# Kernel optimization log

Measured on AMD Instinct MI355X. Metric: run time of the kernel, lower is better.

Reference implementation:

```python
import jax, jax.numpy as jnp
import numpy as np

N, E, G = 50000, 800000, 64
DIN, H, DOUT = 128, 64, 1
T = 3  # AttentiveFP message-passing timesteps
NEG_SLOPE = 0.2


def setup_inputs() -> dict:
    key = jax.random.key(0)
    ks = jax.random.split(key, 16)
    s = 0.05
    return {
        "x": jax.random.normal(ks[0], (N, DIN), jnp.float32),
        "edge_index": jax.random.randint(ks[1], (2, E), 0, N),
        "batch": jnp.sort(jax.random.randint(ks[2], (N,), 0, G)),
        "W_in": jax.random.normal(ks[3], (DIN, H), jnp.float32) * s,
        "b_in": jnp.zeros((H,), jnp.float32),
        "a_att": jax.random.normal(ks[4], (2 * H,), jnp.float32) * s,
        "Wi": jax.random.normal(ks[5], (H, 3 * H), jnp.float32) * s,
        "Wh": jax.random.normal(ks[6], (H, 3 * H), jnp.float32) * s,
        "bi": jnp.zeros((3 * H,), jnp.float32),
        "bh": jnp.zeros((3 * H,), jnp.float32),
        "W1": jax.random.normal(ks[7], (2 * H, H), jnp.float32) * s,
        "b1": jnp.zeros((H,), jnp.float32),
        "W2": jax.random.normal(ks[8], (H, DOUT), jnp.float32) * s,
        "b2": jnp.zeros((DOUT,), jnp.float32),
    }


def _segment_softmax(scores, seg, n):
    m = jax.ops.segment_max(scores, seg, num_segments=n)
    e = jnp.exp(scores - m[seg])
    z = jax.ops.segment_sum(e, seg, num_segments=n)
    return e / (z[seg] + 1e-16)


def reference(x, edge_index, batch, W_in, b_in, a_att, Wi, Wh, bi, bh, W1, b1, W2, b2):
    src, dst = edge_index[0], edge_index[1]
    # input projection
    h = jax.nn.relu(x @ W_in + b_in)  # [N, H]
    for _ in range(T):
        # attention-weighted message passing (AttentiveFP style)
        h_src, h_dst = h[src], h[dst]                      # [E, H] gathers
        score = jax.nn.leaky_relu(
            h_src @ a_att[:H] + h_dst @ a_att[H:], NEG_SLOPE)  # [E]
        alpha = _segment_softmax(score, dst, N)            # softmax over incoming edges
        m = jax.ops.segment_sum(alpha[:, None] * h_src, dst, num_segments=N)  # [N, H]
        # GRU cell update: h = GRU(m, h)
        gi = m @ Wi + bi
        gh = h @ Wh + bh
        r = jax.nn.sigmoid(gi[:, :H] + gh[:, :H])
        z = jax.nn.sigmoid(gi[:, H:2 * H] + gh[:, H:2 * H])
        n = jnp.tanh(gi[:, 2 * H:] + r * gh[:, 2 * H:])
        h = (1.0 - z) * n + z * h
    # graph readout: mean || max pooling -> [G, 2H]
    cnt = jax.ops.segment_sum(jnp.ones((N,), h.dtype), batch, num_segments=G)
    meanp = jax.ops.segment_sum(h, batch, num_segments=G) / jnp.maximum(cnt, 1.0)[:, None]
    maxp = jax.ops.segment_max(h, batch, num_segments=G)
    maxp = jnp.where(jnp.isfinite(maxp), maxp, 0.0)
    g = jnp.concatenate([meanp, maxp], axis=-1)  # [G, 2H]
    # dropout is identity in eval mode; MLP head
    g = jax.nn.relu(g @ W1 + b1)
    return g @ W2 + b2  # [G, DOUT]
```

## Files before the change

kernel.cpp:

```cpp
#include <hip/hip_runtime.h>
#include <math.h>

#define DIN 128
#define HD 64
#define NEG 0.2f

typedef short s16x8 __attribute__((ext_vector_type(8)));
typedef float f32x4 __attribute__((ext_vector_type(4)));

__device__ __forceinline__ float sigmoidf_(float x) { return 1.f / (1.f + __expf(-x)); }
__device__ __forceinline__ float tanhf_(float x)    { return 2.f / (1.f + __expf(-2.f*x)) - 1.f; }

__device__ __forceinline__ void split2(float a, float b, unsigned& dh, unsigned& dl) {
  unsigned ha = __float_as_uint(a) & 0xffff0000u;
  unsigned hb = __float_as_uint(b) & 0xffff0000u;
  float ra = a - __uint_as_float(ha);
  float rb = b - __uint_as_float(hb);
  unsigned la = __float_as_uint(ra) & 0xffff0000u;
  unsigned lb = __float_as_uint(rb) & 0xffff0000u;
  dh = (ha >> 16) | hb;
  dl = (la >> 16) | lb;
}

__device__ __forceinline__ unsigned pack2rne(float a, float b) {
  unsigned ua = __float_as_uint(a); ua += 0x7fffu + ((ua >> 16) & 1u);
  unsigned ub = __float_as_uint(b); ub += 0x7fffu + ((ub >> 16) & 1u);
  return (ua >> 16) | (ub & 0xffff0000u);
}
__device__ __forceinline__ float bflo(unsigned u) { return __uint_as_float(u << 16); }
__device__ __forceinline__ float bfhi(unsigned u) { return __uint_as_float(u & 0xffff0000u); }

__device__ __forceinline__ f32x4 mfma16(uint4 a, uint4 b, f32x4 c) {
  return __builtin_amdgcn_mfma_f32_16x16x32_bf16(
      __builtin_bit_cast(s16x8, a), __builtin_bit_cast(s16x8, b), c, 0, 0, 0);
}

__global__ void k_count(const int* __restrict__ dst, int E, int* __restrict__ deg) {
  int e = blockIdx.x*256 + threadIdx.x;
  if (e < E) atomicAdd(&deg[dst[e]], 1);
}

__global__ void k_scan1(const int* __restrict__ deg, int n, int* __restrict__ rowst, int* __restrict__ bsum) {
  __shared__ int s[256];
  int i = blockIdx.x*256 + threadIdx.x;
  int v = (i < n) ? deg[i] : 0;
  s[threadIdx.x] = v;
  __syncthreads();
  for (int off = 1; off < 256; off <<= 1) {
    int t = (threadIdx.x >= off) ? s[threadIdx.x - off] : 0;
    __syncthreads();
    s[threadIdx.x] += t;
    __syncthreads();
  }
  if (i < n) rowst[i] = s[threadIdx.x] - v;
  if (threadIdx.x == 255) bsum[blockIdx.x] = s[255];
}

__global__ void k_scan2(int* bsum, int nb) {
  __shared__ int s[256];
  int v = (threadIdx.x < nb) ? bsum[threadIdx.x] : 0;
  s[threadIdx.x] = v;
  __syncthreads();
  for (int off = 1; off < 256; off <<= 1) {
    int t = (threadIdx.x >= off) ? s[threadIdx.x - off] : 0;
    __syncthreads();
    s[threadIdx.x] += t;
    __syncthreads();
  }
  if (threadIdx.x < nb) bsum[threadIdx.x] = s[threadIdx.x] - v;
}

__global__ void k_scan3(int* __restrict__ rowst, const int* __restrict__ bsum, int n, int E, int* __restrict__ deg) {
  int i = blockIdx.x*256 + threadIdx.x;
  if (i < n) { rowst[i] += bsum[blockIdx.x]; deg[i] = 0; }
  if (i == 0) rowst[n] = E;
}

__global__ void k_scatter8(const int* __restrict__ src, const int* __restrict__ dst, int E,
                           const int* __restrict__ rowst, int* __restrict__ fill,
                           int* __restrict__ csr, int n) {
  int xcd = blockIdx.x & 7;
  int chunk = blockIdx.x >> 3;
  int nch = gridDim.x >> 3;
  int per = (E + nch - 1) / nch;
  int e0 = chunk * per;
  int e1 = (e0 + per < E) ? e0 + per : E;
  int n8 = (n + 7) >> 3;
  int lo = xcd * n8;
  int hi = (lo + n8 < n) ? lo + n8 : n;
  for (int e = e0 + threadIdx.x; e < e1; e += 256) {
    int d = dst[e];
    if (d >= lo && d < hi) {
      int pos = rowst[d] + atomicAdd(&fill[d], 1);
      csr[pos] = src[e];
    }
  }
}

__global__ void k_wtp(const float* __restrict__ Wi, const float* __restrict__ Wh,
                      const float* __restrict__ bi, const float* __restrict__ bh,
                      unsigned* __restrict__ Bhi, unsigned* __restrict__ Blo,
                      float* __restrict__ bc) {
  int idx = blockIdx.x*256 + threadIdx.x;
  if (idx < 16384) {
    int jd  = idx & 3;
    int l   = (idx >> 2) & 63;
    int ntg = (idx >> 8) & 15;
    int ks  = idx >> 12;
    int g = ntg & 3;
    int j = (ntg >> 2)*16 + (l & 15);
    unsigned dh = 0, dl = 0;
#pragma unroll
    for (int half = 0; half < 2; ++half) {
      int k = ks*32 + (l >> 4)*8 + jd*2 + half;
      float v;
      if (g == 0)      v = (k < 64) ? Wi[k*(3*HD) + j]        : Wh[(k-64)*(3*HD) + j];
      else if (g == 1) v = (k < 64) ? Wi[k*(3*HD) + HD + j]   : Wh[(k-64)*(3*HD) + HD + j];
      else if (g == 2) v = (k < 64) ? Wi[k*(3*HD) + 2*HD + j] : 0.f;
      else             v = (k < 64) ? 0.f                     : Wh[(k-64)*(3*HD) + 2*HD + j];
      unsigned hv = __float_as_uint(v) & 0xffff0000u;
      float rf = v - __uint_as_float(hv);
      unsigned lv = __float_as_uint(rf) & 0xffff0000u;
      dh |= (hv >> 16) << (16*half);
      dl |= (lv >> 16) << (16*half);
    }
    Bhi[idx] = dh;
    Blo[idx] = dl;
  }
  if (idx < 256) {
    int g = idx >> 6, j = idx & 63;
    float v;
    if (g == 0)      v = bi[j] + bh[j];
    else if (g == 1) v = bi[HD + j] + bh[HD + j];
    else if (g == 2) v = bi[2*HD + j];
    else             v = bh[2*HD + j];
    bc[idx] = v;
  }
}

__global__ void __launch_bounds__(256) k_proj2(const float* __restrict__ x, const float* __restrict__ Win,
                       const float* __restrict__ bin, const float* __restrict__ aatt, int n,
                       float* __restrict__ h, unsigned* __restrict__ hb,
                       float* __restrict__ ssrc, float* __restrict__ sdst) {
  __shared__ float A[DIN][32];
  int m_base = blockIdx.x * 32;
  int tx = threadIdx.x;
  {
    int m = tx & 31;
    int kq8 = tx >> 5;
    int node = m_base + m;
    bool valid = node < n;
    const float4* x4 = (const float4*)(x + (size_t)node*DIN);
#pragma unroll
    for (int it = 0; it < 4; ++it) {
      int kq = kq8*4 + it;
      int k0 = kq*4;
      float4 v = make_float4(0.f,0.f,0.f,0.f);
      if (valid) v = x4[kq];
      A[k0+0][m] = v.x; A[k0+1][m] = v.y; A[k0+2][m] = v.z; A[k0+3][m] = v.w;
    }
  }
  __syncthreads();

  int c_idx = tx & 31;
  int m_idx = tx >> 5;
  int c0 = c_idx * 2;
  int m0 = m_idx * 4;

  float acc[4][2];
#pragma unroll
  for (int a = 0; a < 4; ++a) { acc[a][0] = 0.f; acc[a][1] = 0.f; }

#pragma unroll 4
  for (int k = 0; k < DIN; ++k) {
    float2 b = *(const float2*)(Win + k*HD + c0);
    float4 a0 = *(const float4*)(&A[k][m0]);
    float av[4] = {a0.x,a0.y,a0.z,a0.w};
#pragma unroll
    for (int a = 0; a < 4; ++a) { acc[a][0] += av[a]*b.x; acc[a][1] += av[a]*b.y; }
  }

  float b0 = bin[c0], b1 = bin[c0+1];
  float a_s0 = aatt[c0],    a_s1 = aatt[c0+1];
  float a_d0 = aatt[HD+c0], a_d1 = aatt[HD+c0+1];

#pragma unroll
  for (int a = 0; a < 4; ++a) {
    int node = m_base + m0 + a;
    float v0 = fmaxf(acc[a][0] + b0, 0.f);
    float v1 = fmaxf(acc[a][1] + b1, 0.f);
    if (node < n) {
      h[(size_t)node*HD + c0]   = v0;
      h[(size_t)node*HD + c0+1] = v1;
      hb[(size_t)node*32 + c_idx] = pack2rne(v0, v1);
    }
    float ps = v0*a_s0 + v1*a_s1;
    float pd = v0*a_d0 + v1*a_d1;
#pragma unroll
    for (int off = 16; off; off >>= 1) { ps += __shfl_xor(ps, off); pd += __shfl_xor(pd, off); }
    if (c_idx == 0 && node < n) { ssrc[node] = ps; sdst[node] = pd; }
  }
}

__global__ void __launch_bounds__(256, 6) k_step(const float* __restrict__ hc, float* __restrict__ hn_,
                      const unsigned* __restrict__ hbc, unsigned* __restrict__ hbn,
                      const float* __restrict__ ssc, const float* __restrict__ sdc,
                      float* __restrict__ ssn, float* __restrict__ sdn,
                      const int* __restrict__ rowst, const int* __restrict__ csr,
                      const unsigned* __restrict__ Bhi, const unsigned* __restrict__ Blo,
                      const float* __restrict__ bc, const float* __restrict__ aatt, int n) {
  __shared__ float Ash[16][68];
  __shared__ int   Ush[16][68];
  __shared__ float Msh[16][68];
  __shared__ float Hn[16][68];
  int tx = threadIdx.x;
  int m_base = blockIdx.x * 16;
  int g16 = tx >> 4, l16 = tx & 15;

  {
    int node = m_base + g16;
    int s0 = 0, s1 = 0; float sdv = 0.f;
    if (node < n) { s0 = rowst[node]; s1 = rowst[node+1]; sdv = sdc[node]; }
    int deg = s1 - s0;
    float4 acc0 = make_float4(0.f,0.f,0.f,0.f);
    float4 acc1 = make_float4(0.f,0.f,0.f,0.f);
    float4 acc2 = make_float4(0.f,0.f,0.f,0.f);
    float4 acc3 = make_float4(0.f,0.f,0.f,0.f);

    if (deg > 0 && deg <= 64) {
      float mx = -INFINITY;
      float areg[4];
      int   ureg[4];
#pragma unroll
      for (int c = 0; c < 4; ++c) {
        int idx = s0 + c*16 + l16;
        int uu = csr[(idx < s1) ? idx : s0];
        ureg[c] = uu;
        float sc = -INFINITY;
        if (idx < s1) {
          sc = ssc[uu] + sdv;
          sc = (sc > 0.f) ? sc : NEG*sc;
        }
        areg[c] = sc;
        mx = fmaxf(mx, sc);
      }
#pragma unroll
      for (int off = 8; off; off >>= 1) mx = fmaxf(mx, __shfl_xor(mx, off, 16));
      float zs = 0.f;
#pragma unroll
      for (int c = 0; c < 4; ++c) {
        float e = __expf(areg[c] - mx);
        Ash[g16][c*16 + l16] = e;
        Ush[g16][c*16 + l16] = ureg[c];
        zs += e;
      }
#pragma unroll
      for (int off = 8; off; off >>= 1) zs += __shfl_xor(zs, off, 16);
      float zi = 1.f / (zs + 1e-16f);

      for (int c = 0; c < 4; ++c) {
        int base = s0 + c*16;
        if (base >= s1) break;
#pragma unroll
        for (int e0 = 0; e0 < 16; e0 += 4) {
          if (base + e0 < s1) {
            int   u0 = Ush[g16][c*16 + e0 + 0];
            int   u1 = Ush[g16][c*16 + e0 + 1];
            int   u2 = Ush[g16][c*16 + e0 + 2];
            int   u3 = Ush[g16][c*16 + e0 + 3];
            float a0 = Ash[g16][c*16 + e0 + 0];
            float a1 = Ash[g16][c*16 + e0 + 1];
            float a2 = Ash[g16][c*16 + e0 + 2];
            float a3 = Ash[g16][c*16 + e0 + 3];
            uint2 q0 = *((const uint2*)hbc + (size_t)u0*16 + l16);
            uint2 q1 = *((const uint2*)hbc + (size_t)u1*16 + l16);
            uint2 q2 = *((const uint2*)hbc + (size_t)u2*16 + l16);
            uint2 q3 = *((const uint2*)hbc + (size_t)u3*16 + l16);
            acc0.x += a0*bflo(q0.x); acc0.y += a0*bfhi(q0.x); acc0.z += a0*bflo(q0.y); acc0.w += a0*bfhi(q0.y);
            acc1.x += a1*bflo(q1.x); acc1.y += a1*bfhi(q1.x); acc1.z += a1*bflo(q1.y); acc1.w += a1*bfhi(q1.y);
            acc2.x += a2*bflo(q2.x); acc2.y += a2*bfhi(q2.x); acc2.z += a2*bflo(q2.y); acc2.w += a2*bfhi(q2.y);
            acc3.x += a3*bflo(q3.x); acc3.y += a3*bfhi(q3.x); acc3.z += a3*bflo(q3.y); acc3.w += a3*bfhi(q3.y);
          }
        }
      }
      acc0.x = ((acc0.x + acc1.x) + (acc2.x + acc3.x)) * zi;
      acc0.y = ((acc0.y + acc1.y) + (acc2.y + acc3.y)) * zi;
      acc0.z = ((acc0.z + acc1.z) + (acc2.z + acc3.z)) * zi;
      acc0.w = ((acc0.w + acc1.w) + (acc2.w + acc3.w)) * zi;
    } else if (deg > 64) {
      float mx = -INFINITY;
      for (int i = s0 + l16; i < s1; i += 16) {
        float sc = ssc[csr[i]] + sdv;
        sc = (sc > 0.f) ? sc : NEG*sc;
        mx = fmaxf(mx, sc);
      }
#pragma unroll
      for (int off = 8; off; off >>= 1) mx = fmaxf(mx, __shfl_xor(mx, off, 16));
      float zs = 0.f;
      for (int i = s0 + l16; i < s1; i += 16) {
        float sc = ssc[csr[i]] + sdv;
        sc = (sc > 0.f) ? sc : NEG*sc;
        zs += __expf(sc - mx);
      }
#pragma unroll
      for (int off = 8; off; off >>= 1) zs += __shfl_xor(zs, off, 16);
      float zi = 1.f / (zs + 1e-16f);
      for (int i = s0; i < s1; ++i) {
        int u = csr[i];
        float sc = ssc[u] + sdv;
        sc = (sc > 0.f) ? sc : NEG*sc;
        float p = __expf(sc - mx);
        uint2 q = *((const uint2*)hbc + (size_t)u*16 + l16);
        acc0.x += p*bflo(q.x); acc0.y += p*bfhi(q.x); acc0.z += p*bflo(q.y); acc0.w += p*bfhi(q.y);
      }
      acc0.x *= zi; acc0.y *= zi; acc0.z *= zi; acc0.w *= zi;
    }
    *(float4*)(&Msh[g16][l16*4]) = acc0;
  }
  __syncthreads();

  int w = tx >> 6, l = tx & 63;
  int lrow = l & 15, lk = l >> 4;

  f32x4 acc4[4];
#pragma unroll
  for (int nt = 0; nt < 4; ++nt) acc4[nt] = (f32x4){0.f,0.f,0.f,0.f};

#pragma unroll
  for (int ks = 0; ks < 4; ++ks) {
    uint4 ahi, alo;
    {
      float4 v0, v1;
      if (ks < 2) {
        const float* sp = &Msh[lrow][ks*32 + lk*8];
        v0 = *(const float4*)sp;
        v1 = *(const float4*)(sp + 4);
      } else {
        size_t node = (size_t)(m_base + lrow);
        const float* sp = hc + node*HD + (ks-2)*32 + lk*8;
        v0 = *(const float4*)sp;
        v1 = *(const float4*)(sp + 4);
      }
      split2(v0.x, v0.y, ahi.x, alo.x);
      split2(v0.z, v0.w, ahi.y, alo.y);
      split2(v1.x, v1.y, ahi.z, alo.z);
      split2(v1.z, v1.w, ahi.w, alo.w);
    }
#pragma unroll
    for (int nt = 0; nt < 4; ++nt) {
      int ntg = w*4 + nt;
      int fidx = (ks*16 + ntg)*64 + l;
      uint4 bh_ = *((const uint4*)Bhi + fidx);
      uint4 bl_ = *((const uint4*)Blo + fidx);
      acc4[nt] = mfma16(ahi, bh_, acc4[nt]);
      acc4[nt] = mfma16(ahi, bl_, acc4[nt]);
      acc4[nt] = mfma16(alo, bh_, acc4[nt]);
    }
  }

  int j = w*16 + (l & 15);
  float bcr = bc[j], bcz = bc[64 + j], bcg = bc[128 + j], bch = bc[192 + j];
#pragma unroll
  for (int r = 0; r < 4; ++r) {
    int lr = lk*4 + r;
    int noder = m_base + lr;
    float rg = sigmoidf_(acc4[0][r] + bcr);
    float zg = sigmoidf_(acc4[1][r] + bcz);
    float ng = tanhf_(acc4[2][r] + bcg + rg*(acc4[3][r] + bch));
    float hold = (noder < n) ? hc[(size_t)noder*HD + j] : 0.f;
    Hn[lr][j] = (1.f - zg)*ng + zg*hold;
  }
  __syncthreads();

  {
    int node2 = tx >> 4;
    int jb = (tx & 15) * 4;
    float4 h0 = *(const float4*)(&Hn[node2][jb]);
    int gnode = m_base + node2;
    if (gnode < n) {
      *(float4*)(hn_ + (size_t)gnode*HD + jb) = h0;
      ((uint2*)hbn)[(size_t)gnode*16 + (jb >> 2)] =
          make_uint2(pack2rne(h0.x, h0.y), pack2rne(h0.z, h0.w));
    }
    float4 as0 = *(const float4*)(aatt + jb);
    float4 ad0 = *(const float4*)(aatt + HD + jb);
    float ps = h0.x*as0.x + h0.y*as0.y + h0.z*as0.z + h0.w*as0.w;
    float pd = h0.x*ad0.x + h0.y*ad0.y + h0.z*ad0.z + h0.w*ad0.w;
#pragma unroll
    for (int off = 8; off; off >>= 1) { ps += __shfl_xor(ps, off, 16); pd += __shfl_xor(pd, off, 16); }
    if ((tx & 15) == 0 && gnode < n) { ssn[gnode] = ps; sdn[gnode] = pd; }
  }
}

__device__ __forceinline__ int lower_bound_i(const int* a, int n, int key) {
  int lo = 0, hi = n;
  while (lo < hi) { int mid = (lo + hi) >> 1; if (a[mid] < key) lo = mid + 1; else hi = mid; }
  return lo;
}

__global__ void k_pool1(const float* __restrict__ h, const int* __restrict__ batch, int n,
                        float* __restrict__ psum, float* __restrict__ pmax) {
  int g = blockIdx.x >> 3, slice = blockIdx.x & 7;
  int lane = threadIdx.x;
  int lo = lower_bound_i(batch, n, g);
  int hi = lower_bound_i(batch, n, g + 1);
  int span = hi - lo;
  int s0 = lo + (int)(((long long)span * slice) >> 3);
  int s1 = lo + (int)(((long long)span * (slice + 1)) >> 3);
  float sum0 = 0.f, sum1 = 0.f, sum2 = 0.f, sum3 = 0.f;
  float mx0 = -INFINITY, mx1 = -INFINITY, mx2 = -INFINITY, mx3 = -INFINITY;
  int i = s0;
  for (; i + 3 < s1; i += 4) {
    float v0 = h[(size_t)(i+0)*HD + lane];
    float v1 = h[(size_t)(i+1)*HD + lane];
    float v2 = h[(size_t)(i+2)*HD + lane];
    float v3 = h[(size_t)(i+3)*HD + lane];
    sum0 += v0; sum1 += v1; sum2 += v2; sum3 += v3;
    mx0 = fmaxf(mx0, v0); mx1 = fmaxf(mx1, v1); mx2 = fmaxf(mx2, v2); mx3 = fmaxf(mx3, v3);
  }
  for (; i < s1; ++i) {
    float v = h[(size_t)i*HD + lane];
    sum0 += v; mx0 = fmaxf(mx0, v);
  }
  float sum = (sum0 + sum1) + (sum2 + sum3);
  float mx = fmaxf(fmaxf(mx0, mx1), fmaxf(mx2, mx3));
  psum[(size_t)blockIdx.x*HD + lane] = sum;
  pmax[(size_t)blockIdx.x*HD + lane] = mx;
}

__global__ void k_pool2(const float* __restrict__ psum, const float* __restrict__ pmax,
                        const int* __restrict__ batch, int n, float* __restrict__ gpool) {
  int g = blockIdx.x;
  int lane = threadIdx.x;
  int lo = lower_bound_i(batch, n, g);
  int hi = lower_bound_i(batch, n, g + 1);
  int cnt = hi - lo;
  float sum = 0.f, mx = -INFINITY;
#pragma unroll
  for (int s = 0; s < 8; ++s) {
    sum += psum[(size_t)(g*8+s)*HD + lane];
    mx = fmaxf(mx, pmax[(size_t)(g*8+s)*HD + lane]);
  }
  float mean = sum / fmaxf((float)cnt, 1.f);
  if (cnt <= 0 || !isfinite(mx)) mx = 0.f;
  gpool[(size_t)g*2*HD + lane] = mean;
  gpool[(size_t)g*2*HD + HD + lane] = mx;
}

__global__ void k_head(const float* __restrict__ gpool, const float* __restrict__ W1,
                       const float* __restrict__ b1, const float* __restrict__ W2,
                       const float* __restrict__ b2, float* __restrict__ out) {
  int g = blockIdx.x, j = threadIdx.x;
  const float* gr = gpool + (size_t)g*2*HD;
  float acc = b1[j];
#pragma unroll
  for (int k = 0; k < 2*HD; ++k) acc += gr[k] * W1[k*HD + j];
  acc = fmaxf(acc, 0.f);
  float v = acc * W2[j];
#pragma unroll
  for (int off = 32; off; off >>= 1) v += __shfl_xor(v, off);
  if (j == 0) out[g] = v + b2[0];
}

extern "C" void kernel_launch(void* const* d_in, const int* in_sizes, int n_in,
                              void* d_out, int out_size, void* d_ws, size_t ws_size,
                              hipStream_t stream) {
  const float* x     = (const float*)d_in[0];
  const int*   ei    = (const int*)d_in[1];
  const int*   batch = (const int*)d_in[2];
  const float* Win   = (const float*)d_in[3];
  const float* bin   = (const float*)d_in[4];
  const float* aatt  = (const float*)d_in[5];
  const float* Wi    = (const float*)d_in[6];
  const float* Wh    = (const float*)d_in[7];
  const float* bi    = (const float*)d_in[8];
  const float* bh    = (const float*)d_in[9];
  const float* W1    = (const float*)d_in[10];
  const float* b1    = (const float*)d_in[11];
  const float* W2    = (const float*)d_in[12];
  const float* b2    = (const float*)d_in[13];
  float* out = (float*)d_out;

  int N = in_sizes[0] / DIN;
  int E = in_sizes[1] / 2;
  int G = out_size;

  const int* srcp = ei;
  const int* dstp = ei + E;

  char* base = (char*)d_ws;
  size_t off = 0;
  auto alloc = [&](size_t bytes) -> char* {
    char* p = base + off;
    off += (bytes + 255) & ~(size_t)255;
    return p;
  };
  float* h0    = (float*)alloc((size_t)N*HD*4);
  float* h1    = (float*)alloc((size_t)N*HD*4);
  unsigned* hb0 = (unsigned*)alloc((size_t)N*32*4);
  unsigned* hb1 = (unsigned*)alloc((size_t)N*32*4);
  float* ssrc0 = (float*)alloc((size_t)N*4);
  float* ssrc1 = (float*)alloc((size_t)N*4);
  float* sdst0 = (float*)alloc((size_t)N*4);
  float* sdst1 = (float*)alloc((size_t)N*4);
  int*   deg   = (int*)  alloc((size_t)N*4);
  int*   rowst = (int*)  alloc((size_t)(N+1)*4);
  int*   csr   = (int*)  alloc((size_t)E*4);
  unsigned* Bhi = (unsigned*)alloc((size_t)16384*4);
  unsigned* Blo = (unsigned*)alloc((size_t)16384*4);
  float* bc    = (float*)alloc((size_t)256*4);
  float* gpool = (float*)alloc((size_t)G*2*HD*4);
  float* psum  = (float*)alloc((size_t)G*8*HD*4);
  float* pmax  = (float*)alloc((size_t)G*8*HD*4);
  int*   bsum  = (int*)  alloc(1024);
  (void)ws_size; (void)n_in;

  int nbN = (N + 255)/256, nbE = (E + 255)/256;

  hipMemsetAsync(deg, 0, (size_t)N*4, stream);
  k_count<<<nbE, 256, 0, stream>>>(dstp, E, deg);
  k_scan1<<<nbN, 256, 0, stream>>>(deg, N, rowst, bsum);
  k_scan2<<<1, 256, 0, stream>>>(bsum, nbN);
  k_scan3<<<nbN, 256, 0, stream>>>(rowst, bsum, N, E, deg);
  k_scatter8<<<2048, 256, 0, stream>>>(srcp, dstp, E, rowst, deg, csr, N);
  k_wtp<<<64, 256, 0, stream>>>(Wi, Wh, bi, bh, Bhi, Blo, bc);
  k_proj2<<<(N + 31)/32, 256, 0, stream>>>(x, Win, bin, aatt, N, h0, hb0, ssrc0, sdst0);

  float* hc = h0;  float* hn = h1;
  unsigned* hbc = hb0; unsigned* hbn = hb1;
  float* ssc = ssrc0; float* sdc = sdst0;
  float* ssn = ssrc1; float* sdn = sdst1;
  for (int t = 0; t < 3; ++t) {
    k_step<<<(N + 15)/16, 256, 0, stream>>>(hc, hn, hbc, hbn, ssc, sdc, ssn, sdn,
                                            rowst, csr, Bhi, Blo, bc, aatt, N);
    float* tmp;
    unsigned* utmp;
    tmp = hc; hc = hn; hn = tmp;
    utmp = hbc; hbc = hbn; hbn = utmp;
    tmp = ssc; ssc = ssn; ssn = tmp;
    tmp = sdc; sdc = sdn; sdn = tmp;
  }
  k_pool1<<<G*8, 64, 0, stream>>>(hc, batch, N, psum, pmax);
  k_pool2<<<G, 64, 0, stream>>>(psum, pmax, batch, N, gpool);
  k_head<<<G, 64, 0, stream>>>(gpool, W1, b1, W2, b2, out);
}
```

Before: 280.1 us.

## Merge prep kernels into one launch, fuse scan stages and pool with head

The count, weight-pack and input-projection kernels become a single launch that branches on block index. The two scan fix-up kernels become one, where each block sums the earlier block totals itself. The pool-finalise and MLP head kernels are also fused, with shared memory replacing the gpool buffer. The step kernel's launch bounds rise from 6 to 8 blocks per SM. The aim is to cut launch overhead and small serial kernels, at the cost of redundant prefix summing per block and possible register spills in the step kernel.

Result: faster. 262.3 us (-6.4%).

```diff
diff --git a/kernel.cpp b/kernel.cpp
--- a/kernel.cpp
+++ b/kernel.cpp
@@ -35,9 +35,115 @@
       __builtin_bit_cast(s16x8, a), __builtin_bit_cast(s16x8, b), c, 0, 0, 0);
 }
 
-__global__ void k_count(const int* __restrict__ dst, int E, int* __restrict__ deg) {
-  int e = blockIdx.x*256 + threadIdx.x;
-  if (e < E) atomicAdd(&deg[dst[e]], 1);
+__global__ void __launch_bounds__(256) k_prep(
+    const float* __restrict__ x, const float* __restrict__ Win,
+    const float* __restrict__ bin, const float* __restrict__ aatt, int n,
+    float* __restrict__ h, unsigned* __restrict__ hb,
+    float* __restrict__ ssrc, float* __restrict__ sdst, int nbP,
+    const int* __restrict__ dst, int E, int* __restrict__ deg, int nbE,
+    const float* __restrict__ Wi, const float* __restrict__ Wh,
+    const float* __restrict__ bi, const float* __restrict__ bh,
+    unsigned* __restrict__ Bhi, unsigned* __restrict__ Blo, float* __restrict__ bc) {
+  int bid = blockIdx.x;
+  int tx = threadIdx.x;
+  if (bid < nbP) {
+    __shared__ float A[DIN][32];
+    int m_base = bid * 32;
+    {
+      int m = tx & 31;
+      int kq8 = tx >> 5;
+      int node = m_base + m;
+      bool valid = node < n;
+      const float4* x4 = (const float4*)(x + (size_t)node*DIN);
+#pragma unroll
+      for (int it = 0; it < 4; ++it) {
+        int kq = kq8*4 + it;
+        int k0 = kq*4;
+        float4 v = make_float4(0.f,0.f,0.f,0.f);
+        if (valid) v = x4[kq];
+        A[k0+0][m] = v.x; A[k0+1][m] = v.y; A[k0+2][m] = v.z; A[k0+3][m] = v.w;
+      }
+    }
+    __syncthreads();
+
+    int c_idx = tx & 31;
+    int m_idx = tx >> 5;
+    int c0 = c_idx * 2;
+    int m0 = m_idx * 4;
+
+    float acc[4][2];
+#pragma unroll
+    for (int a = 0; a < 4; ++a) { acc[a][0] = 0.f; acc[a][1] = 0.f; }
+
+#pragma unroll 4
+    for (int k = 0; k < DIN; ++k) {
+      float2 b = *(const float2*)(Win + k*HD + c0);
+      float4 a0 = *(const float4*)(&A[k][m0]);
+      float av[4] = {a0.x,a0.y,a0.z,a0.w};
+#pragma unroll
+      for (int a = 0; a < 4; ++a) { acc[a][0] += av[a]*b.x; acc[a][1] += av[a]*b.y; }
+    }
+
+    float b0 = bin[c0], b1 = bin[c0+1];
+    float a_s0 = aatt[c0],    a_s1 = aatt[c0+1];
+    float a_d0 = aatt[HD+c0], a_d1 = aatt[HD+c0+1];
+
+#pragma unroll
+    for (int a = 0; a < 4; ++a) {
+      int node = m_base + m0 + a;
+      float v0 = fmaxf(acc[a][0] + b0, 0.f);
+      float v1 = fmaxf(acc[a][1] + b1, 0.f);
+      if (node < n) {
+        h[(size_t)node*HD + c0]   = v0;
+        h[(size_t)node*HD + c0+1] = v1;
+        hb[(size_t)node*32 + c_idx] = pack2rne(v0, v1);
+      }
+      float ps = v0*a_s0 + v1*a_s1;
+      float pd = v0*a_d0 + v1*a_d1;
+#pragma unroll
+      for (int off = 16; off; off >>= 1) { ps += __shfl_xor(ps, off); pd += __shfl_xor(pd, off); }
+      if (c_idx == 0 && node < n) { ssrc[node] = ps; sdst[node] = pd; }
+    }
+  } else if (bid < nbP + nbE) {
+    int e = (bid - nbP)*256 + tx;
+    if (e < E) atomicAdd(&deg[dst[e]], 1);
+  } else {
+    int idx = (bid - nbP - nbE)*256 + tx;
+    if (idx < 16384) {
+      int jd  = idx & 3;
+      int l   = (idx >> 2) & 63;
+      int ntg = (idx >> 8) & 15;
+      int ks  = idx >> 12;
+      int g = ntg & 3;
+      int j = (ntg >> 2)*16 + (l & 15);
+      unsigned dh = 0, dl = 0;
+#pragma unroll
+      for (int half = 0; half < 2; ++half) {
+        int k = ks*32 + (l >> 4)*8 + jd*2 + half;
+        float v;
+        if (g == 0)      v = (k < 64) ? Wi[k*(3*HD) + j]        : Wh[(k-64)*(3*HD) + j];
+        else if (g == 1) v = (k < 64) ? Wi[k*(3*HD) + HD + j]   : Wh[(k-64)*(3*HD) + HD + j];
+        else if (g == 2) v = (k < 64) ? Wi[k*(3*HD) + 2*HD + j] : 0.f;
+        else             v = (k < 64) ? 0.f                     : Wh[(k-64)*(3*HD) + 2*HD + j];
+        unsigned hv = __float_as_uint(v) & 0xffff0000u;
+        float rf = v - __uint_as_float(hv);
+        unsigned lv = __float_as_uint(rf) & 0xffff0000u;
+        dh |= (hv >> 16) << (16*half);
+        dl |= (lv >> 16) << (16*half);
+      }
+      Bhi[idx] = dh;
+      Blo[idx] = dl;
+    }
+    if (idx < 256) {
+      int g = idx >> 6, j = idx & 63;
+      float v;
+      if (g == 0)      v = bi[j] + bh[j];
+      else if (g == 1) v = bi[HD + j] + bh[HD + j];
+      else if (g == 2) v = bi[2*HD + j];
+      else             v = bh[2*HD + j];
+      bc[idx] = v;
+    }
+  }
 }
 
 __global__ void k_scan1(const int* __restrict__ deg, int n, int* __restrict__ rowst, int* __restrict__ bsum) {
@@ -56,23 +162,20 @@
   if (threadIdx.x == 255) bsum[blockIdx.x] = s[255];
 }
 
-__global__ void k_scan2(int* bsum, int nb) {
-  __shared__ int s[256];
-  int v = (threadIdx.x < nb) ? bsum[threadIdx.x] : 0;
-  s[threadIdx.x] = v;
+__global__ void k_scan23(int* __restrict__ rowst, const int* __restrict__ bsum,
+                         int n, int E, int* __restrict__ deg) {
+  __shared__ int warp_s[4];
+  __shared__ int pref_s;
+  int partial = 0;
+  for (int i = threadIdx.x; i < (int)blockIdx.x; i += 256) partial += bsum[i];
+#pragma unroll
+  for (int off = 32; off; off >>= 1) partial += __shfl_xor(partial, off);
+  if ((threadIdx.x & 63) == 0) warp_s[threadIdx.x >> 6] = partial;
   __syncthreads();
-  for (int off = 1; off < 256; off <<= 1) {
-    int t = (threadIdx.x >= off) ? s[threadIdx.x - off] : 0;
-    __syncthreads();
-    s[threadIdx.x] += t;
-    __syncthreads();
-  }
-  if (threadIdx.x < nb) bsum[threadIdx.x] = s[threadIdx.x] - v;
-}
-
-__global__ void k_scan3(int* __restrict__ rowst, const int* __restrict__ bsum, int n, int E, int* __restrict__ deg) {
+  if (threadIdx.x == 0) pref_s = warp_s[0] + warp_s[1] + warp_s[2] + warp_s[3];
+  __syncthreads();
   int i = blockIdx.x*256 + threadIdx.x;
-  if (i < n) { rowst[i] += bsum[blockIdx.x]; deg[i] = 0; }
+  if (i < n) { rowst[i] += pref_s; deg[i] = 0; }
   if (i == 0) rowst[n] = E;
 }
 
@@ -97,112 +200,7 @@
   }
 }
 
-__global__ void k_wtp(const float* __restrict__ Wi, const float* __restrict__ Wh,
-                      const float* __restrict__ bi, const float* __restrict__ bh,
-                      unsigned* __restrict__ Bhi, unsigned* __restrict__ Blo,
-                      float* __restrict__ bc) {
-  int idx = blockIdx.x*256 + threadIdx.x;
-  if (idx < 16384) {
-    int jd  = idx & 3;
-    int l   = (idx >> 2) & 63;
-    int ntg = (idx >> 8) & 15;
-    int ks  = idx >> 12;
-    int g = ntg & 3;
-    int j = (ntg >> 2)*16 + (l & 15);
-    unsigned dh = 0, dl = 0;
-#pragma unroll
-    for (int half = 0; half < 2; ++half) {
-      int k = ks*32 + (l >> 4)*8 + jd*2 + half;
-      float v;
-      if (g == 0)      v = (k < 64) ? Wi[k*(3*HD) + j]        : Wh[(k-64)*(3*HD) + j];
-      else if (g == 1) v = (k < 64) ? Wi[k*(3*HD) + HD + j]   : Wh[(k-64)*(3*HD) + HD + j];
-      else if (g == 2) v = (k < 64) ? Wi[k*(3*HD) + 2*HD + j] : 0.f;
-      else             v = (k < 64) ? 0.f                     : Wh[(k-64)*(3*HD) + 2*HD + j];
-      unsigned hv = __float_as_uint(v) & 0xffff0000u;
-      float rf = v - __uint_as_float(hv);
-      unsigned lv = __float_as_uint(rf) & 0xffff0000u;
-      dh |= (hv >> 16) << (16*half);
-      dl |= (lv >> 16) << (16*half);
-    }
-    Bhi[idx] = dh;
-    Blo[idx] = dl;
-  }
-  if (idx < 256) {
-    int g = idx >> 6, j = idx & 63;
-    float v;
-    if (g == 0)      v = bi[j] + bh[j];
-    else if (g == 1) v = bi[HD + j] + bh[HD + j];
-    else if (g == 2) v = bi[2*HD + j];
-    else             v = bh[2*HD + j];
-    bc[idx] = v;
-  }
-}
-
-__global__ void __launch_bounds__(256) k_proj2(const float* __restrict__ x, const float* __restrict__ Win,
-                       const float* __restrict__ bin, const float* __restrict__ aatt, int n,
-                       float* __restrict__ h, unsigned* __restrict__ hb,
-                       float* __restrict__ ssrc, float* __restrict__ sdst) {
-  __shared__ float A[DIN][32];
-  int m_base = blockIdx.x * 32;
-  int tx = threadIdx.x;
-  {
-    int m = tx & 31;
-    int kq8 = tx >> 5;
-    int node = m_base + m;
-    bool valid = node < n;
-    const float4* x4 = (const float4*)(x + (size_t)node*DIN);
-#pragma unroll
-    for (int it = 0; it < 4; ++it) {
-      int kq = kq8*4 + it;
-      int k0 = kq*4;
-      float4 v = make_float4(0.f,0.f,0.f,0.f);
-      if (valid) v = x4[kq];
-      A[k0+0][m] = v.x; A[k0+1][m] = v.y; A[k0+2][m] = v.z; A[k0+3][m] = v.w;
-    }
-  }
-  __syncthreads();
-
-  int c_idx = tx & 31;
-  int m_idx = tx >> 5;
-  int c0 = c_idx * 2;
-  int m0 = m_idx * 4;
-
-  float acc[4][2];
-#pragma unroll
-  for (int a = 0; a < 4; ++a) { acc[a][0] = 0.f; acc[a][1] = 0.f; }
-
-#pragma unroll 4
-  for (int k = 0; k < DIN; ++k) {
-    float2 b = *(const float2*)(Win + k*HD + c0);
-    float4 a0 = *(const float4*)(&A[k][m0]);
-    float av[4] = {a0.x,a0.y,a0.z,a0.w};
-#pragma unroll
-    for (int a = 0; a < 4; ++a) { acc[a][0] += av[a]*b.x; acc[a][1] += av[a]*b.y; }
-  }
-
-  float b0 = bin[c0], b1 = bin[c0+1];
-  float a_s0 = aatt[c0],    a_s1 = aatt[c0+1];
-  float a_d0 = aatt[HD+c0], a_d1 = aatt[HD+c0+1];
-
-#pragma unroll
-  for (int a = 0; a < 4; ++a) {
-    int node = m_base + m0 + a;
-    float v0 = fmaxf(acc[a][0] + b0, 0.f);
-    float v1 = fmaxf(acc[a][1] + b1, 0.f);
-    if (node < n) {
-      h[(size_t)node*HD + c0]   = v0;
-      h[(size_t)node*HD + c0+1] = v1;
-      hb[(size_t)node*32 + c_idx] = pack2rne(v0, v1);
-    }
-    float ps = v0*a_s0 + v1*a_s1;
-    float pd = v0*a_d0 + v1*a_d1;
-#pragma unroll
-    for (int off = 16; off; off >>= 1) { ps += __shfl_xor(ps, off); pd += __shfl_xor(pd, off); }
-    if (c_idx == 0 && node < n) { ssrc[node] = ps; sdst[node] = pd; }
-  }
-}
-
-__global__ void __launch_bounds__(256, 6) k_step(const float* __restrict__ hc, float* __restrict__ hn_,
+__global__ void __launch_bounds__(256, 8) k_step(const float* __restrict__ hc, float* __restrict__ hn_,
                       const unsigned* __restrict__ hbc, unsigned* __restrict__ hbn,
                       const float* __restrict__ ssc, const float* __restrict__ sdc,
                       float* __restrict__ ssn, float* __restrict__ sdn,
@@ -428,8 +426,11 @@
   pmax[(size_t)blockIdx.x*HD + lane] = mx;
 }
 
-__global__ void k_pool2(const float* __restrict__ psum, const float* __restrict__ pmax,
-                        const int* __restrict__ batch, int n, float* __restrict__ gpool) {
+__global__ void k_poolhead(const float* __restrict__ psum, const float* __restrict__ pmax,
+                           const int* __restrict__ batch, int n,
+                           const float* __restrict__ W1, const float* __restrict__ b1,
+                           const float* __restrict__ W2, const float* __restrict__ b2,
+                           float* __restrict__ out) {
   int g = blockIdx.x;
   int lane = threadIdx.x;
   int lo = lower_bound_i(batch, n, g);
@@ -443,23 +444,18 @@
   }
   float mean = sum / fmaxf((float)cnt, 1.f);
   if (cnt <= 0 || !isfinite(mx)) mx = 0.f;
-  gpool[(size_t)g*2*HD + lane] = mean;
-  gpool[(size_t)g*2*HD + HD + lane] = mx;
-}
-
-__global__ void k_head(const float* __restrict__ gpool, const float* __restrict__ W1,
-                       const float* __restrict__ b1, const float* __restrict__ W2,
-                       const float* __restrict__ b2, float* __restrict__ out) {
-  int g = blockIdx.x, j = threadIdx.x;
-  const float* gr = gpool + (size_t)g*2*HD;
-  float acc = b1[j];
-#pragma unroll
-  for (int k = 0; k < 2*HD; ++k) acc += gr[k] * W1[k*HD + j];
+  __shared__ float gr[2*HD];
+  gr[lane] = mean;
+  gr[HD + lane] = mx;
+  __syncthreads();
+  float acc = b1[lane];
+#pragma unroll
+  for (int k = 0; k < 2*HD; ++k) acc += gr[k] * W1[k*HD + lane];
   acc = fmaxf(acc, 0.f);
-  float v = acc * W2[j];
+  float v = acc * W2[lane];
 #pragma unroll
   for (int off = 32; off; off >>= 1) v += __shfl_xor(v, off);
-  if (j == 0) out[g] = v + b2[0];
+  if (lane == 0) out[g] = v + b2[0];
 }
 
 extern "C" void kernel_launch(void* const* d_in, const int* in_sizes, int n_in,
@@ -509,22 +505,21 @@
   unsigned* Bhi = (unsigned*)alloc((size_t)16384*4);
   unsigned* Blo = (unsigned*)alloc((size_t)16384*4);
   float* bc    = (float*)alloc((size_t)256*4);
-  float* gpool = (float*)alloc((size_t)G*2*HD*4);
   float* psum  = (float*)alloc((size_t)G*8*HD*4);
   float* pmax  = (float*)alloc((size_t)G*8*HD*4);
   int*   bsum  = (int*)  alloc(1024);
   (void)ws_size; (void)n_in;
 
   int nbN = (N + 255)/256, nbE = (E + 255)/256;
+  int nbP = (N + 31)/32;
 
   hipMemsetAsync(deg, 0, (size_t)N*4, stream);
-  k_count<<<nbE, 256, 0, stream>>>(dstp, E, deg);
+  k_prep<<<nbP + nbE + 64, 256, 0, stream>>>(x, Win, bin, aatt, N, h0, hb0, ssrc0, sdst0, nbP,
+                                             dstp, E, deg, nbE,
+                                             Wi, Wh, bi, bh, Bhi, Blo, bc);
   k_scan1<<<nbN, 256, 0, stream>>>(deg, N, rowst, bsum);
-  k_scan2<<<1, 256, 0, stream>>>(bsum, nbN);
-  k_scan3<<<nbN, 256, 0, stream>>>(rowst, bsum, N, E, deg);
+  k_scan23<<<nbN, 256, 0, stream>>>(rowst, bsum, N, E, deg);
   k_scatter8<<<2048, 256, 0, stream>>>(srcp, dstp, E, rowst, deg, csr, N);
-  k_wtp<<<64, 256, 0, stream>>>(Wi, Wh, bi, bh, Bhi, Blo, bc);
-  k_proj2<<<(N + 31)/32, 256, 0, stream>>>(x, Win, bin, aatt, N, h0, hb0, ssrc0, sdst0);
 
   float* hc = h0;  float* hn = h1;
   unsigned* hbc = hb0; unsigned* hbn = hb1;
@@ -541,6 +536,5 @@
     tmp = sdc; sdc = sdn; sdn = tmp;
   }
   k_pool1<<<G*8, 64, 0, stream>>>(hc, batch, N, psum, pmax);
-  k_pool2<<<G, 64, 0, stream>>>(psum, pmax, batch, N, gpool);
-  k_head<<<G, 64, 0, stream>>>(gpool, W1, b1, W2, b2, out);
-}
+  k_poolhead<<<G, 64, 0, stream>>>(psum, pmax, batch, N, W1, b1, W2, b2, out);
+}
```
